# Performance work log

Measured on AMD Instinct MI355X. Metric: run time of the kernel, lower is better.

Reference implementation:

```python
import jax, jax.numpy as jnp
import numpy as np

N = 200000
E = 6400000
IN_F = 128
HID = 128
OUT_F = 16
LAYERS = 3
EPS = 1e-5


def setup_inputs() -> dict:
    key = jax.random.key(0)
    ks = jax.random.split(key, 12)
    nodes = jax.random.normal(ks[0], (N, IN_F), dtype=jnp.float32)
    src = jax.random.randint(ks[1], (E,), 0, N, dtype=jnp.int32)
    dst = jax.random.randint(ks[2], (E,), 0, N, dtype=jnp.int32)
    s_in = 1.0 / np.sqrt(IN_F)
    s_h = 1.0 / np.sqrt(HID)
    W_in = jax.random.uniform(ks[3], (IN_F, HID), jnp.float32, -s_in, s_in)
    b_in = jax.random.uniform(ks[4], (HID,), jnp.float32, -s_in, s_in)
    Ws = jax.random.uniform(ks[5], (LAYERS, HID, HID), jnp.float32, -s_h, s_h)
    bs = jax.random.uniform(ks[6], (LAYERS, HID), jnp.float32, -s_h, s_h)
    gammas = jnp.ones((LAYERS, HID), jnp.float32)
    betas = jnp.zeros((LAYERS, HID), jnp.float32)
    W_out = jax.random.uniform(ks[7], (HID, OUT_F), jnp.float32, -s_h, s_h)
    b_out = jax.random.uniform(ks[8], (OUT_F,), jnp.float32, -s_h, s_h)
    return {"nodes": nodes, "src": src, "dst": dst, "W_in": W_in, "b_in": b_in,
            "Ws": Ws, "bs": bs, "gammas": gammas, "betas": betas,
            "W_out": W_out, "b_out": b_out}


def _layernorm(x, g, b):
    mu = jnp.mean(x, axis=-1, keepdims=True)
    var = jnp.var(x, axis=-1, keepdims=True)
    return (x - mu) * jax.lax.rsqrt(var + EPS) * g + b


def reference(nodes, src, dst, W_in, b_in, Ws, bs, gammas, betas, W_out, b_out):
    # in-degree for 'gcn' aggregator normalization: (sum_neigh + self) / (deg + 1)
    deg = jax.ops.segment_sum(jnp.ones((E,), jnp.float32), dst, num_segments=N)
    inv = 1.0 / (deg + 1.0)  # [N]
    x = nodes @ W_in + b_in  # [N, HID]
    for l in range(LAYERS):
        agg = jax.ops.segment_sum(x[src], dst, num_segments=N)  # gather+scatter-add
        h = (agg + x) * inv[:, None]          # gcn mean incl. self
        h = h @ Ws[l] + bs[l]                 # fc_neigh
        h = jax.nn.relu(h)                    # activation (before norm, per DGL)
        x = _layernorm(h, gammas[l], betas[l])
    return x @ W_out + b_out  # [N, OUT_F]
```

## Files before the change

### kernel.cpp

```cpp
#include <hip/hip_runtime.h>

#define N_NODES 200000
#define N_EDGES 6400000
#define HID 128
#define OUTF 16
#define LAYERS 3
#define EPS 1e-5f

#define NRANGES 16
#define RANGE_N 12500
#define NBUCKETS 800
#define BUCKET_N 250
#define BATCH 5000
#define NBATCH (N_EDGES / BATCH)
#define RCAP 405000
#define RBLK (RCAP / BATCH)
#define BCAP 9500

typedef unsigned int u32;

__device__ __forceinline__ unsigned short f2bf(float f){
  unsigned int u = __float_as_uint(f);
  u += 0x7fffu + ((u >> 16) & 1u);
  return (unsigned short)(u >> 16);
}
__device__ __forceinline__ u32 pack2bf(float lo, float hi){
  return (u32)f2bf(lo) | ((u32)f2bf(hi) << 16);
}


__global__ __launch_bounds__(256) void k_initcur(int* __restrict__ range_cursor,
                                                 int* __restrict__ bucket_cursor){
  int t = blockIdx.x * 256 + threadIdx.x;
  if (t < NRANGES) range_cursor[t] = t * RCAP;
  if (t < NBUCKETS) bucket_cursor[t] = t * BCAP;
}


__global__ __launch_bounds__(256) void k_p1(const int* __restrict__ src, const int* __restrict__ dst,
                                            int* __restrict__ range_cursor, u32* __restrict__ ebuf1){
  __shared__ u32 stage[BATCH];
  __shared__ int hist[NRANGES], hist2[NRANGES], hbase[NRANGES], gbase[NRANGES];
  const int tid = threadIdx.x;
  const long e0 = (long)blockIdx.x * BATCH;

  if (tid < NRANGES){ hist[tid] = 0; hist2[tid] = 0; }
  __syncthreads();
  for (int i = tid; i < BATCH; i += 256){
    int d = dst[e0 + i];
    atomicAdd(&hist[d / RANGE_N], 1);
  }
  __syncthreads();
  if (tid == 0){ int run = 0; for (int b = 0; b < NRANGES; b++){ hbase[b] = run; run += hist[b]; } }
  __syncthreads();
  if (tid < NRANGES && hist[tid] > 0) gbase[tid] = atomicAdd(&range_cursor[tid], hist[tid]);
  __syncthreads();
  for (int i = tid; i < BATCH; i += 256){
    int d = dst[e0 + i];
    int s = src[e0 + i];
    int r = d / RANGE_N;
    u32 pk = ((u32)(d - r * RANGE_N) << 18) | (u32)s;
    int p = atomicAdd(&hist2[r], 1);
    stage[hbase[r] + p] = pk;
  }
  __syncthreads();
  for (int b = 0; b < NRANGES; b++){
    int len = hist[b];
    int gb = gbase[b], hb = hbase[b];
    for (int i = tid; i < len; i += 256) ebuf1[gb + i] = stage[hb + i];
  }
}


__global__ __launch_bounds__(256) void k_p2(const u32* __restrict__ ebuf1, const int* __restrict__ range_cursor,
                                            int* __restrict__ bucket_cursor, u32* __restrict__ ebuf2){
  __shared__ u32 stage[BATCH];
  __shared__ int hist[50], hist2[50], hbase[50], gbase[50];
  const int tid = threadIdx.x;
  const int r = blockIdx.x / RBLK;
  const int chunk = blockIdx.x % RBLK;
  const int rlen = range_cursor[r] - r * RCAP;
  const int i0 = chunk * BATCH;
  const int len = min(BATCH, rlen - i0);
  if (len <= 0) return;
  const u32* seg = ebuf1 + (long)r * RCAP + i0;

  if (tid < 50){ hist[tid] = 0; hist2[tid] = 0; }
  __syncthreads();
  for (int i = tid; i < len; i += 256){
    int dl = (int)(seg[i] >> 18);
    atomicAdd(&hist[dl / BUCKET_N], 1);
  }
  __syncthreads();
  if (tid == 0){ int run = 0; for (int b = 0; b < 50; b++){ hbase[b] = run; run += hist[b]; } }
  __syncthreads();
  if (tid < 50 && hist[tid] > 0) gbase[tid] = atomicAdd(&bucket_cursor[r * 50 + tid], hist[tid]);
  __syncthreads();
  for (int i = tid; i < len; i += 256){
    u32 pk = seg[i];
    int b = (int)(pk >> 18) / BUCKET_N;
    int p = atomicAdd(&hist2[b], 1);
    stage[hbase[b] + p] = pk;
  }
  __syncthreads();
  for (int b = 0; b < 50; b++){
    int l = hist[b];
    if (l == 0) continue;
    int gb = gbase[b], hb = hbase[b];
    for (int i = tid; i < l; i += 256) ebuf2[gb + i] = stage[hb + i];
  }
}


__global__ __launch_bounds__(256) void k_scanb(const int* __restrict__ bucket_cursor,
                                               int* __restrict__ bucket_base){
  __shared__ int q[256];
  int tid = threadIdx.x;
  int v[4]; int sum4 = 0;
  if (tid < 200){
    #pragma unroll
    for (int j = 0; j < 4; j++){ int b = 4 * tid + j; v[j] = bucket_cursor[b] - b * BCAP; sum4 += v[j]; }
  }
  q[tid] = sum4; __syncthreads();
  for (int off = 1; off < 256; off <<= 1){
    int t = (tid >= off) ? q[tid - off] : 0;
    __syncthreads();
    q[tid] += t;
    __syncthreads();
  }
  if (tid < 200){
    int run = q[tid] - sum4;
    #pragma unroll
    for (int j = 0; j < 4; j++){ bucket_base[4 * tid + j] = run; run += v[j]; }
  }
}


__global__ __launch_bounds__(256) void k_p3(const u32* __restrict__ ebuf2, const int* __restrict__ bucket_cursor,
                                            const int* __restrict__ bucket_base,
                                            int* __restrict__ csr, int* __restrict__ row_start){
  __shared__ int stage[BCAP];
  __shared__ int hist[BUCKET_N], sbase[BUCKET_N], cur[BUCKET_N];
  __shared__ int q[256];
  const int tid = threadIdx.x;
  const int b = blockIdx.x;
  const int n0 = b * BUCKET_N;
  const int dl0 = (b % 50) * BUCKET_N;
  const int len = min(bucket_cursor[b] - b * BCAP, BCAP);
  const int base = bucket_base[b];
  const u32* seg = ebuf2 + (long)b * BCAP;

  if (tid < BUCKET_N){ hist[tid] = 0; cur[tid] = 0; }
  __syncthreads();
  for (int i = tid; i < len; i += 256){
    int local = (int)(seg[i] >> 18) - dl0;
    local = min(max(local, 0), BUCKET_N - 1);
    atomicAdd(&hist[local], 1);
  }
  __syncthreads();
  {
    int v = (tid < BUCKET_N) ? hist[tid] : 0;
    q[tid] = v; __syncthreads();
    for (int off = 1; off < 256; off <<= 1){
      int t = (tid >= off) ? q[tid - off] : 0;
      __syncthreads();
      q[tid] += t;
      __syncthreads();
    }
    if (tid < BUCKET_N) sbase[tid] = q[tid] - v;
  }
  __syncthreads();
  for (int i = tid; i < len; i += 256){
    u32 pk = seg[i];
    int local = (int)(pk >> 18) - dl0;
    local = min(max(local, 0), BUCKET_N - 1);
    int pos = atomicAdd(&cur[local], 1);
    stage[sbase[local] + pos] = (int)(pk & 0x3FFFFu);
  }
  __syncthreads();
  for (int i = tid; i < len; i += 256) csr[base + i] = stage[i];
  if (tid < BUCKET_N) row_start[n0 + tid] = base + sbase[tid];
  if (b == NBUCKETS - 1 && tid == 0) row_start[N_NODES] = base + len;
}


__global__ __launch_bounds__(256) void k_gemm128(const float* __restrict__ A,
    const float* __restrict__ W, const float* __restrict__ bias,
    float* __restrict__ xout, u32* __restrict__ xbout)
{
  __shared__ float As[64][132];
  const int tid = threadIdx.x;
  const long row0 = (long)blockIdx.x * 64;

  const float4* A4 = (const float4*)(A + row0 * HID);
  for (int i = tid; i < 64 * 32; i += 256){
    int r = i >> 5, c = i & 31;
    *(float4*)&As[r][c * 4] = A4[r * 32 + c];
  }
  __syncthreads();

  const int cg = tid & 31;
  const int rg = tid >> 5;
  const int c0 = cg * 4;
  float acc[8][4];
  {
    float4 b = *(const float4*)&bias[c0];
    #pragma unroll
    for (int r = 0; r < 8; r++){ acc[r][0]=b.x; acc[r][1]=b.y; acc[r][2]=b.z; acc[r][3]=b.w; }
  }

  for (int k = 0; k < HID; k += 4){
    float4 w0 = *(const float4*)&W[(k + 0) * HID + c0];
    float4 w1 = *(const float4*)&W[(k + 1) * HID + c0];
    float4 w2 = *(const float4*)&W[(k + 2) * HID + c0];
    float4 w3 = *(const float4*)&W[(k + 3) * HID + c0];
    #pragma unroll
    for (int r = 0; r < 8; r++){
      float4 a = *(const float4*)&As[rg * 8 + r][k];
      acc[r][0] = fmaf(a.w, w3.x, fmaf(a.z, w2.x, fmaf(a.y, w1.x, fmaf(a.x, w0.x, acc[r][0]))));
      acc[r][1] = fmaf(a.w, w3.y, fmaf(a.z, w2.y, fmaf(a.y, w1.y, fmaf(a.x, w0.y, acc[r][1]))));
      acc[r][2] = fmaf(a.w, w3.z, fmaf(a.z, w2.z, fmaf(a.y, w1.z, fmaf(a.x, w0.z, acc[r][2]))));
      acc[r][3] = fmaf(a.w, w3.w, fmaf(a.z, w2.w, fmaf(a.y, w1.w, fmaf(a.x, w0.w, acc[r][3]))));
    }
  }

  #pragma unroll
  for (int r = 0; r < 8; r++){
    long row = row0 + rg * 8 + r;
    float4 v; v.x = acc[r][0]; v.y = acc[r][1]; v.z = acc[r][2]; v.w = acc[r][3];
    *(float4*)&xout[row * HID + c0] = v;
    uint2 p; p.x = pack2bf(v.x, v.y); p.y = pack2bf(v.z, v.w);
    *(uint2*)&xbout[(row * HID + c0) >> 1] = p;
  }
}


__global__ __launch_bounds__(256) void k_fused(const int* __restrict__ row_start,
    const int* __restrict__ csr, const uint2* __restrict__ xb2,
    const float* __restrict__ x_old,
    const float* __restrict__ W, const float* __restrict__ bias,
    const float* __restrict__ gamma, const float* __restrict__ beta,
    float* __restrict__ xout, u32* __restrict__ xbout)
{
  __shared__ float As[64][132];
  __shared__ float part[64][4][2];
  __shared__ float mu_s[64], rs_s[64];
  __shared__ float gam_s[128], bet_s[128];
  const int tid = threadIdx.x;
  const long row0 = (long)blockIdx.x * 64;

  if (tid < 128){ gam_s[tid] = gamma[tid]; bet_s[tid] = beta[tid]; }

  {
    const int wv = tid >> 6;
    const int lane = tid & 63;
    const int half = lane >> 5, col = lane & 31;
    const uint2* xbc = xb2 + col;

    for (int i = 0; i < 16; i++){
      const int r = wv * 16 + i;
      const int node = (int)row0 + r;
      const int s0 = row_start[node], s1 = row_start[node + 1];

      float4 xs = {0.f, 0.f, 0.f, 0.f};
      if (half == 0) xs = *(const float4*)&x_old[(long)node * HID + col * 4];

      float a0 = 0.f, a1 = 0.f, a2 = 0.f, a3 = 0.f;
      int base = s0;
      int idx[8];
      if (base + 16 <= s1){
        #pragma unroll
        for (int j = 0; j < 8; j++) idx[j] = csr[base + 2*j + half];
      }
      while (base + 16 <= s1){
        uint2 p[8];
        #pragma unroll
        for (int j = 0; j < 8; j++) p[j] = xbc[(long)idx[j] * 32];
        base += 16;
        if (base + 16 <= s1){
          #pragma unroll
          for (int j = 0; j < 8; j++) idx[j] = csr[base + 2*j + half];
        }
        #pragma unroll
        for (int j = 0; j < 8; j++){
          a0 += __uint_as_float(p[j].x << 16);
          a1 += __uint_as_float(p[j].x & 0xffff0000u);
          a2 += __uint_as_float(p[j].y << 16);
          a3 += __uint_as_float(p[j].y & 0xffff0000u);
        }
      }
      if (base < s1){
        const int s1m1 = s1 - 1;
        int ti[8];
        #pragma unroll
        for (int j = 0; j < 8; j++) ti[j] = csr[min(base + 2*j + half, s1m1)];
        uint2 p[8];
        #pragma unroll
        for (int j = 0; j < 8; j++) p[j] = xbc[(long)ti[j] * 32];
        #pragma unroll
        for (int j = 0; j < 8; j++){
          bool act = (base + 2*j + half) < s1;
          float v0 = __uint_as_float(p[j].x << 16);
          float v1 = __uint_as_float(p[j].x & 0xffff0000u);
          float v2 = __uint_as_float(p[j].y << 16);
          float v3 = __uint_as_float(p[j].y & 0xffff0000u);
          a0 += act ? v0 : 0.f;
          a1 += act ? v1 : 0.f;
          a2 += act ? v2 : 0.f;
          a3 += act ? v3 : 0.f;
        }
      }

      a0 += __shfl_down(a0, 32);
      a1 += __shfl_down(a1, 32);
      a2 += __shfl_down(a2, 32);
      a3 += __shfl_down(a3, 32);

      if (half == 0){
        float inv = 1.f / (float)(s1 - s0 + 1);
        float4 rv;
        rv.x = (a0 + xs.x) * inv;
        rv.y = (a1 + xs.y) * inv;
        rv.z = (a2 + xs.z) * inv;
        rv.w = (a3 + xs.w) * inv;
        *(float4*)&As[r][col * 4] = rv;
      }
    }
  }
  __syncthreads();

  const int cg = tid & 31;
  const int rg = tid >> 5;
  const int c0 = cg * 4;
  float acc[8][4];
  {
    float4 b = *(const float4*)&bias[c0];
    #pragma unroll
    for (int r = 0; r < 8; r++){ acc[r][0]=b.x; acc[r][1]=b.y; acc[r][2]=b.z; acc[r][3]=b.w; }
  }

  for (int k = 0; k < HID; k += 4){
    float4 w0 = *(const float4*)&W[(k + 0) * HID + c0];
    float4 w1 = *(const float4*)&W[(k + 1) * HID + c0];
    float4 w2 = *(const float4*)&W[(k + 2) * HID + c0];
    float4 w3 = *(const float4*)&W[(k + 3) * HID + c0];
    #pragma unroll
    for (int r = 0; r < 8; r++){
      float4 a = *(const float4*)&As[rg * 8 + r][k];
      acc[r][0] = fmaf(a.w, w3.x, fmaf(a.z, w2.x, fmaf(a.y, w1.x, fmaf(a.x, w0.x, acc[r][0]))));
      acc[r][1] = fmaf(a.w, w3.y, fmaf(a.z, w2.y, fmaf(a.y, w1.y, fmaf(a.x, w0.y, acc[r][1]))));
      acc[r][2] = fmaf(a.w, w3.z, fmaf(a.z, w2.z, fmaf(a.y, w1.z, fmaf(a.x, w0.z, acc[r][2]))));
      acc[r][3] = fmaf(a.w, w3.w, fmaf(a.z, w2.w, fmaf(a.y, w1.w, fmaf(a.x, w0.w, acc[r][3]))));
    }
  }

  __syncthreads();
  #pragma unroll
  for (int r = 0; r < 8; r++){
    float4 v;
    v.x = fmaxf(acc[r][0], 0.f); v.y = fmaxf(acc[r][1], 0.f);
    v.z = fmaxf(acc[r][2], 0.f); v.w = fmaxf(acc[r][3], 0.f);
    *(float4*)&As[rg * 8 + r][c0] = v;
  }
  __syncthreads();
  {
    int row = tid >> 2, qq = tid & 3;
    float s = 0.f, s2 = 0.f;
    #pragma unroll 8
    for (int c = 0; c < 32; c++){ float v = As[row][qq * 32 + c]; s += v; s2 += v * v; }
    part[row][qq][0] = s; part[row][qq][1] = s2;
  }
  __syncthreads();
  if (tid < 64){
    float s  = part[tid][0][0] + part[tid][1][0] + part[tid][2][0] + part[tid][3][0];
    float s2 = part[tid][0][1] + part[tid][1][1] + part[tid][2][1] + part[tid][3][1];
    float mu = s * (1.f / HID);
    float var = s2 * (1.f / HID) - mu * mu;
    mu_s[tid] = mu;
    rs_s[tid] = 1.f / sqrtf(var + EPS);
  }
  __syncthreads();
  for (int i = tid; i < 64 * 32; i += 256){
    int r = i >> 5, c4 = (i & 31) * 4;
    float4 v = *(float4*)&As[r][c4];
    float mu = mu_s[r], rs = rs_s[r];
    v.x = (v.x - mu) * rs * gam_s[c4 + 0] + bet_s[c4 + 0];
    v.y = (v.y - mu) * rs * gam_s[c4 + 1] + bet_s[c4 + 1];
    v.z = (v.z - mu) * rs * gam_s[c4 + 2] + bet_s[c4 + 2];
    v.w = (v.w - mu) * rs * gam_s[c4 + 3] + bet_s[c4 + 3];
    long row = row0 + r;
    *(float4*)&xout[row * HID + c4] = v;
    uint2 p; p.x = pack2bf(v.x, v.y); p.y = pack2bf(v.z, v.w);
    *(uint2*)&xbout[(row * HID + c4) >> 1] = p;
  }
}


__global__ __launch_bounds__(256) void k_gemm_out(const float* __restrict__ x,
    const float* __restrict__ Wo, const float* __restrict__ bo, float* __restrict__ out)
{
  __shared__ float As[16][132];
  __shared__ float Wl[HID * OUTF];
  const int tid = threadIdx.x;
  const long row0 = (long)blockIdx.x * 16;
  const float4* A4 = (const float4*)(x + row0 * HID);
  for (int i = tid; i < 16 * 32; i += 256){
    int r = i >> 5, c = i & 31;
    *(float4*)&As[r][c * 4] = A4[r * 32 + c];
  }
  for (int i = tid; i < HID * OUTF; i += 256) Wl[i] = Wo[i];
  __syncthreads();
  int col = tid & 15, r = tid >> 4;
  float acc = bo[col];
  for (int k = 0; k < HID; k += 4){
    float4 a = *(const float4*)&As[r][k];
    acc = fmaf(a.x, Wl[(k + 0) * OUTF + col],
          fmaf(a.y, Wl[(k + 1) * OUTF + col],
          fmaf(a.z, Wl[(k + 2) * OUTF + col],
          fmaf(a.w, Wl[(k + 3) * OUTF + col], acc))));
  }
  out[(row0 + r) * OUTF + col] = acc;
}


extern "C" void kernel_launch(void* const* d_in, const int* in_sizes, int n_in,
                              void* d_out, int out_size, void* d_ws, size_t ws_size,
                              hipStream_t stream)
{
  (void)in_sizes; (void)n_in; (void)out_size; (void)ws_size;
  const float* nodes = (const float*)d_in[0];
  const int*   src   = (const int*)d_in[1];
  const int*   dst   = (const int*)d_in[2];
  const float* W_in  = (const float*)d_in[3];
  const float* b_in  = (const float*)d_in[4];
  const float* Ws    = (const float*)d_in[5];
  const float* bs    = (const float*)d_in[6];
  const float* gam   = (const float*)d_in[7];
  const float* bet   = (const float*)d_in[8];
  const float* W_out = (const float*)d_in[9];
  const float* b_out = (const float*)d_in[10];
  float* out = (float*)d_out;

  size_t off = 0;
  auto bump = [&](size_t bytes) -> char* {
    char* p = (char*)d_ws + off;
    off = (off + bytes + 255) & ~(size_t)255;
    return p;
  };
  int* row_start     = (int*)bump((N_NODES + 1) * sizeof(int));
  int* range_cursor  = (int*)bump(NRANGES * sizeof(int));
  int* bucket_cursor = (int*)bump(NBUCKETS * sizeof(int));
  int* bucket_base   = (int*)bump((NBUCKETS + 1) * sizeof(int));
  int* csr           = (int*)bump((size_t)N_EDGES * sizeof(int));
  float* x0          = (float*)bump((size_t)N_NODES * HID * sizeof(float));
  float* x1          = (float*)bump((size_t)N_NODES * HID * sizeof(float));
  u32* xb0           = (u32*)bump((size_t)N_NODES * HID * sizeof(unsigned short));
  u32* xb1           = (u32*)bump((size_t)N_NODES * HID * sizeof(unsigned short));

  u32* ebuf1 = (u32*)x0;
  u32* ebuf2 = (u32*)x1;

  k_initcur<<<4, 256, 0, stream>>>(range_cursor, bucket_cursor);
  k_p1<<<NBATCH, 256, 0, stream>>>(src, dst, range_cursor, ebuf1);
  k_p2<<<NRANGES * RBLK, 256, 0, stream>>>(ebuf1, range_cursor, bucket_cursor, ebuf2);
  k_scanb<<<1, 256, 0, stream>>>(bucket_cursor, bucket_base);
  k_p3<<<NBUCKETS, 256, 0, stream>>>(ebuf2, bucket_cursor, bucket_base, csr, row_start);

  k_gemm128<<<N_NODES / 64, 256, 0, stream>>>(nodes, W_in, b_in, x0, xb0);

  const float* xi = x0;  float* xo = x1;
  const u32*   xbi = xb0; u32*  xbo = xb1;
  for (int l = 0; l < LAYERS; l++){
    k_fused<<<N_NODES / 64, 256, 0, stream>>>(row_start, csr, (const uint2*)xbi, xi,
                                              Ws + (size_t)l * HID * HID, bs + l * HID,
                                              gam + l * HID, bet + l * HID, xo, xbo);
    const float* tx = xi; xi = xo; xo = (float*)tx;
    const u32* tb = xbi; xbi = xbo; xbo = (u32*)tb;
  }

  k_gemm_out<<<N_NODES / 16, 256, 0, stream>>>(xi, W_out, b_out, out);
}
```

Baseline: 1.401 ms.

## Halve fused layer tile and do LayerNorm stats with warp shuffles

```diff
diff --git a/kernel.cpp b/kernel.cpp
--- a/kernel.cpp
+++ b/kernel.cpp
@@ -16,6 +16,8 @@
 #define RCAP 405000
 #define RBLK (RCAP / BATCH)
 #define BCAP 9500
+
+#define FTILE 32
 
 typedef unsigned int u32;
 
@@ -242,14 +244,9 @@
     const float* __restrict__ gamma, const float* __restrict__ beta,
     float* __restrict__ xout, u32* __restrict__ xbout)
 {
-  __shared__ float As[64][132];
-  __shared__ float part[64][4][2];
-  __shared__ float mu_s[64], rs_s[64];
-  __shared__ float gam_s[128], bet_s[128];
-  const int tid = threadIdx.x;
-  const long row0 = (long)blockIdx.x * 64;
-
-  if (tid < 128){ gam_s[tid] = gamma[tid]; bet_s[tid] = beta[tid]; }
+  __shared__ float As[FTILE][132];
+  const int tid = threadIdx.x;
+  const long row0 = (long)blockIdx.x * FTILE;
 
   {
     const int wv = tid >> 6;
@@ -257,8 +254,8 @@
     const int half = lane >> 5, col = lane & 31;
     const uint2* xbc = xb2 + col;
 
-    for (int i = 0; i < 16; i++){
-      const int r = wv * 16 + i;
+    for (int i = 0; i < FTILE / 4; i++){
+      const int r = wv * (FTILE / 4) + i;
       const int node = (int)row0 + r;
       const int s0 = row_start[node], s1 = row_start[node + 1];
 
@@ -332,11 +329,11 @@
   const int cg = tid & 31;
   const int rg = tid >> 5;
   const int c0 = cg * 4;
-  float acc[8][4];
+  float acc[4][4];
   {
     float4 b = *(const float4*)&bias[c0];
     #pragma unroll
-    for (int r = 0; r < 8; r++){ acc[r][0]=b.x; acc[r][1]=b.y; acc[r][2]=b.z; acc[r][3]=b.w; }
+    for (int r = 0; r < 4; r++){ acc[r][0]=b.x; acc[r][1]=b.y; acc[r][2]=b.z; acc[r][3]=b.w; }
   }
 
   for (int k = 0; k < HID; k += 4){
@@ -345,8 +342,8 @@
     float4 w2 = *(const float4*)&W[(k + 2) * HID + c0];
     float4 w3 = *(const float4*)&W[(k + 3) * HID + c0];
     #pragma unroll
-    for (int r = 0; r < 8; r++){
-      float4 a = *(const float4*)&As[rg * 8 + r][k];
+    for (int r = 0; r < 4; r++){
+      float4 a = *(const float4*)&As[rg * 4 + r][k];
       acc[r][0] = fmaf(a.w, w3.x, fmaf(a.z, w2.x, fmaf(a.y, w1.x, fmaf(a.x, w0.x, acc[r][0]))));
       acc[r][1] = fmaf(a.w, w3.y, fmaf(a.z, w2.y, fmaf(a.y, w1.y, fmaf(a.x, w0.y, acc[r][1]))));
       acc[r][2] = fmaf(a.w, w3.z, fmaf(a.z, w2.z, fmaf(a.y, w1.z, fmaf(a.x, w0.z, acc[r][2]))));
@@ -354,44 +351,42 @@
     }
   }
 
-  __syncthreads();
+  float s[4], s2[4];
   #pragma unroll
-  for (int r = 0; r < 8; r++){
+  for (int r = 0; r < 4; r++){
+    float v0 = fmaxf(acc[r][0], 0.f);
+    float v1 = fmaxf(acc[r][1], 0.f);
+    float v2 = fmaxf(acc[r][2], 0.f);
+    float v3 = fmaxf(acc[r][3], 0.f);
+    acc[r][0] = v0; acc[r][1] = v1; acc[r][2] = v2; acc[r][3] = v3;
+    s[r]  = (v0 + v1) + (v2 + v3);
+    s2[r] = fmaf(v0, v0, fmaf(v1, v1, fmaf(v2, v2, v3 * v3)));
+  }
+  #pragma unroll
+  for (int m = 1; m < 32; m <<= 1){
+    #pragma unroll
+    for (int r = 0; r < 4; r++){
+      s[r]  += __shfl_xor(s[r],  m);
+      s2[r] += __shfl_xor(s2[r], m);
+    }
+  }
+
+  const float4 gm = *(const float4*)&gamma[c0];
+  const float4 bt = *(const float4*)&beta[c0];
+  #pragma unroll
+  for (int r = 0; r < 4; r++){
+    float mu = s[r] * (1.f / HID);
+    float var = s2[r] * (1.f / HID) - mu * mu;
+    float rs = 1.f / sqrtf(var + EPS);
     float4 v;
-    v.x = fmaxf(acc[r][0], 0.f); v.y = fmaxf(acc[r][1], 0.f);
-    v.z = fmaxf(acc[r][2], 0.f); v.w = fmaxf(acc[r][3], 0.f);
-    *(float4*)&As[rg * 8 + r][c0] = v;
-  }
-  __syncthreads();
-  {
-    int row = tid >> 2, qq = tid & 3;
-    float s = 0.f, s2 = 0.f;
-    #pragma unroll 8
-    for (int c = 0; c < 32; c++){ float v = As[row][qq * 32 + c]; s += v; s2 += v * v; }
-    part[row][qq][0] = s; part[row][qq][1] = s2;
-  }
-  __syncthreads();
-  if (tid < 64){
-    float s  = part[tid][0][0] + part[tid][1][0] + part[tid][2][0] + part[tid][3][0];
-    float s2 = part[tid][0][1] + part[tid][1][1] + part[tid][2][1] + part[tid][3][1];
-    float mu = s * (1.f / HID);
-    float var = s2 * (1.f / HID) - mu * mu;
-    mu_s[tid] = mu;
-    rs_s[tid] = 1.f / sqrtf(var + EPS);
-  }
-  __syncthreads();
-  for (int i = tid; i < 64 * 32; i += 256){
-    int r = i >> 5, c4 = (i & 31) * 4;
-    float4 v = *(float4*)&As[r][c4];
-    float mu = mu_s[r], rs = rs_s[r];
-    v.x = (v.x - mu) * rs * gam_s[c4 + 0] + bet_s[c4 + 0];
-    v.y = (v.y - mu) * rs * gam_s[c4 + 1] + bet_s[c4 + 1];
-    v.z = (v.z - mu) * rs * gam_s[c4 + 2] + bet_s[c4 + 2];
-    v.w = (v.w - mu) * rs * gam_s[c4 + 3] + bet_s[c4 + 3];
-    long row = row0 + r;
-    *(float4*)&xout[row * HID + c4] = v;
+    v.x = (acc[r][0] - mu) * rs * gm.x + bt.x;
+    v.y = (acc[r][1] - mu) * rs * gm.y + bt.y;
+    v.z = (acc[r][2] - mu) * rs * gm.z + bt.z;
+    v.w = (acc[r][3] - mu) * rs * gm.w + bt.w;
+    long row = row0 + rg * 4 + r;
+    *(float4*)&xout[row * HID + c0] = v;
     uint2 p; p.x = pack2bf(v.x, v.y); p.y = pack2bf(v.z, v.w);
-    *(uint2*)&xbout[(row * HID + c4) >> 1] = p;
+    *(uint2*)&xbout[(row * HID + c0) >> 1] = p;
   }
 }
 
@@ -471,9 +466,9 @@
   const float* xi = x0;  float* xo = x1;
   const u32*   xbi = xb0; u32*  xbo = xb1;
   for (int l = 0; l < LAYERS; l++){
-    k_fused<<<N_NODES / 64, 256, 0, stream>>>(row_start, csr, (const uint2*)xbi, xi,
-                                              Ws + (size_t)l * HID * HID, bs + l * HID,
-                                              gam + l * HID, bet + l * HID, xo, xbo);
+    k_fused<<<N_NODES / FTILE, 256, 0, stream>>>(row_start, csr, (const uint2*)xbi, xi,
+                                                 Ws + (size_t)l * HID * HID, bs + l * HID,
+                                                 gam + l * HID, bet + l * HID, xo, xbo);
     const float* tx = xi; xi = xo; xo = (float*)tx;
     const u32* tb = xbi; xbi = xbo; xbo = (u32*)tb;
   }
```

Result: faster. 1.358 ms (-3.1%).
